# Kernel tuning notes

Hardware: AMD Instinct MI355X
Metric: run time of the kernel (lower is better)

The kernel has to match this reference:

```python
import jax, jax.numpy as jnp
import numpy as np

T = 256          # total_sequence_length
COND = 192       # condition_size
H = 256          # latent_size
B = 4096         # batch
MEAN = 0.0
STD = 1.0


def setup_inputs() -> dict:
    key = jax.random.key(0)
    ks = jax.random.split(key, 8)
    s = 1.0 / np.sqrt(H)  # PyTorch RNN init scale
    return {
        "cd": jax.random.normal(ks[0], (B, COND), dtype=jnp.float32),
        "prediction": jax.random.normal(ks[1], (B, T - COND), dtype=jnp.float32),
        "w_ih": jax.random.uniform(ks[2], (4 * H, 1), jnp.float32, -s, s),
        "w_hh": jax.random.uniform(ks[3], (4 * H, H), jnp.float32, -s, s),
        "b_ih": jax.random.uniform(ks[4], (4 * H,), jnp.float32, -s, s),
        "b_hh": jax.random.uniform(ks[5], (4 * H,), jnp.float32, -s, s),
        "w_out": jax.random.uniform(ks[6], (1, H), jnp.float32, -s, s),
        "b_out": jax.random.uniform(ks[7], (1,), jnp.float32, -s, s),
    }


def reference(cd, prediction, w_ih, w_hh, b_ih, b_hh, w_out, b_out):
    # concat condition + prediction -> [B, T], normalize
    d_input = jnp.concatenate([cd, prediction.reshape(-1, T - COND)], axis=1)
    d_input = (d_input - MEAN) / STD
    # time-major [T, B]; input_size=1 so x-projection is an outer product
    x = d_input.T  # [T, B]
    # precompute input gates for all timesteps: [T, B, 4H]
    x_gates = x[:, :, None] * w_ih[:, 0][None, None, :] + b_ih

    def step(carry, xg):
        h, c = carry
        gates = xg + h @ w_hh.T + b_hh  # [B, 4H]
        i, f, g, o = jnp.split(gates, 4, axis=1)
        i = jax.nn.sigmoid(i)
        f = jax.nn.sigmoid(f)
        g = jnp.tanh(g)
        o = jax.nn.sigmoid(o)
        c = f * c + i * g
        h = o * jnp.tanh(c)
        return (h, c), None

    h0 = jnp.zeros((B, H), dtype=cd.dtype)
    c0 = jnp.zeros((B, H), dtype=cd.dtype)
    (h_last, _), _ = jax.lax.scan(step, (h0, c0), x_gates)
    # trailing linear + sigmoid on last hidden state -> [B, 1]
    return jax.nn.sigmoid(h_last @ w_out.T + b_out)
```

## Files before the change

kernel.cpp:

```cpp
#include <hip/hip_runtime.h>

#define TT 256
#define CONDL 192
#define PREDL 64
#define HH 256
#define BB 4096
#define BT 16
#define NTHR 1024

#define WSC 2032.0f
#define HSC 127.0f
#define SINV (1.0f / (127.0f * 2032.0f))
#define L2E 1.44269504f
#define CSX (-L2E * SINV)
#define CGX (2.0f * L2E * SINV)

typedef int i32x4 __attribute__((ext_vector_type(4)));
typedef signed char i8x16 __attribute__((ext_vector_type(16)));
typedef unsigned short u16x4 __attribute__((ext_vector_type(4)));

__device__ __forceinline__ short f2bf(float f) {
  unsigned u = __builtin_bit_cast(unsigned, f);
  unsigned r = (u + 0x7fffu + ((u >> 16) & 1u)) >> 16;
  return (short)r;
}
__device__ __forceinline__ float bf2f(short s) {
  unsigned u = ((unsigned)(unsigned short)s) << 16;
  return __builtin_bit_cast(float, u);
}
__device__ __forceinline__ float sig_(float x) {
  return __builtin_amdgcn_rcpf(1.0f + __builtin_amdgcn_exp2f(-L2E * x));
}

__global__ void pack_w(const float* __restrict__ w_hh, signed char* __restrict__ wq) {
  int idx = blockIdx.x * 256 + threadIdx.x;
  int lane = idx & 63;
  int kb = (idx >> 6) & 3;
  int jt = idx >> 8;
  int n = jt * 16 + (lane & 15);
  int k0 = kb * 64 + (lane >> 4) * 16;
  i8x16 v;
#pragma unroll
  for (int j = 0; j < 16; ++j)
    v[j] = (signed char)__float2int_rn(w_hh[n * 256 + k0 + j] * WSC);
  *(i8x16*)(wq + (long)idx * 16) = v;
}

__global__ __launch_bounds__(NTHR, 4)
void lstm_main(const float* __restrict__ cd, const float* __restrict__ pred,
               const float* __restrict__ w_ih, const float* __restrict__ b_ih,
               const float* __restrict__ b_hh, const float* __restrict__ w_out,
               const float* __restrict__ b_out, const signed char* __restrict__ wq,
               float* __restrict__ out) {
  __shared__ __align__(16) signed char h_s[2 * 4096];
  __shared__ __align__(16) short x_s[TT * BT];

  const int tid = threadIdx.x;
  const int lane = tid & 63;
  const int wv = tid >> 6;
  const int r0 = blockIdx.x * BT;
  const int lm = lane & 15;
  const int lq = lane >> 4;
  const int m0 = lq * 4;

  for (int i = tid; i < BT * CONDL; i += NTHR) {
    int r = i / CONDL, t = i % CONDL;
    x_s[t * BT + r] = f2bf(cd[(r0 + r) * CONDL + t]);
  }
  for (int i = tid; i < BT * PREDL; i += NTHR) {
    int r = i / PREDL, t = i % PREDL;
    x_s[(CONDL + t) * BT + r] = f2bf(pred[(r0 + r) * PREDL + t]);
  }
  for (int i = tid; i < 1024; i += NTHR) ((int*)h_s)[i] = 0;

  const i32x4* wq4 = (const i32x4*)wq;
  i32x4 wrq[16];
#pragma unroll
  for (int g = 0; g < 4; ++g) {
    int jt = g * 16 + wv;
#pragma unroll
    for (int kb = 0; kb < 4; ++kb)
      wrq[g * 4 + kb] = wq4[(jt * 4 + kb) * 64 + lane];
  }
#pragma unroll
  for (int i = 0; i < 16; ++i) asm volatile("" : "+v"(wrq[i]));

  float wf_[4], bf_[4];
#pragma unroll
  for (int g = 0; g < 4; ++g) {
    int j = g * 256 + wv * 16 + lm;
    float fac = (g == 2) ? (2.0f * L2E) : -L2E;
    wf_[g] = w_ih[j] * fac;
    bf_[g] = (b_ih[j] + b_hh[j]) * fac;
  }

  const int wbb = (wv >> 2) * 1024 + (wv & 3) * 256 + lq * 64 + lm;

  float cst[4];
#pragma unroll
  for (int i = 0; i < 4; ++i) cst[i] = 0.f;

  i32x4 zeroi;
  zeroi[0] = 0; zeroi[1] = 0; zeroi[2] = 0; zeroi[3] = 0;

  __syncthreads();

  for (int t = 0; t < TT; ++t) {
    const signed char* hr = h_s + (t & 1) * 4096;
    signed char* hw = h_s + ((t + 1) & 1) * 4096;

    i32x4 acc[4];

    i32x4 af_c = *(const i32x4*)(hr + lane * 16);
#pragma unroll
    for (int kb = 0; kb < 4; ++kb) {
      i32x4 af = af_c;
      if (kb < 3) af_c = *(const i32x4*)(hr + (kb + 1) * 1024 + lane * 16);
      acc[0] = __builtin_amdgcn_mfma_i32_16x16x64_i8(
          af, wrq[0 * 4 + kb], kb ? acc[0] : zeroi, 0, 0, 0);
      acc[1] = __builtin_amdgcn_mfma_i32_16x16x64_i8(
          af, wrq[1 * 4 + kb], kb ? acc[1] : zeroi, 0, 0, 0);
      acc[2] = __builtin_amdgcn_mfma_i32_16x16x64_i8(
          af, wrq[2 * 4 + kb], kb ? acc[2] : zeroi, 0, 0, 0);
      acc[3] = __builtin_amdgcn_mfma_i32_16x16x64_i8(
          af, wrq[3 * 4 + kb], kb ? acc[3] : zeroi, 0, 0, 0);
    }

    u16x4 xq = *(const u16x4*)(x_s + t * BT + m0);
    float xr[4];
#pragma unroll
    for (int v = 0; v < 4; ++v) xr[v] = bf2f((short)xq[v]);

#pragma unroll
    for (int v = 0; v < 4; ++v) {
      float aI = (float)acc[0][v];
      float aF = (float)acc[1][v];
      float aG = (float)acc[2][v];
      float aO = (float)acc[3][v];
      float xi = xr[v];
      float eI = __builtin_amdgcn_exp2f(fmaf(aI, CSX, fmaf(xi, wf_[0], bf_[0])));
      float eF = __builtin_amdgcn_exp2f(fmaf(aF, CSX, fmaf(xi, wf_[1], bf_[1])));
      float eG = __builtin_amdgcn_exp2f(fmaf(aG, CGX, fmaf(xi, wf_[2], bf_[2])));
      float eO = __builtin_amdgcn_exp2f(fmaf(aO, CSX, fmaf(xi, wf_[3], bf_[3])));
      float A_ = 1.0f + eI, F_ = 1.0f + eF, G_ = 1.0f + eG, O_ = 1.0f + eO;
      float AG = A_ * G_;
      float num = fmaf(G_ - 2.0f, F_, cst[v] * AG);
      float r1 = __builtin_amdgcn_rcpf(F_ * AG);
      float cn = num * r1;
      cst[v] = cn;
      float eC = __builtin_amdgcn_exp2f(fminf(cn * (2.0f * L2E), 126.0f));
      float C2 = 1.0f + eC;
      float r2 = __builtin_amdgcn_rcpf(O_ * C2);
      float h127 = fmaf(HSC, C2, -2.0f * HSC) * r2;
      hw[wbb + v * 16] = (signed char)__float2int_rn(h127);
    }
    __syncthreads();
  }

  const signed char* hf = h_s;
  float bo = b_out[0];
  {
    int row = wv;
    float p = 0.f;
#pragma unroll
    for (int c = 0; c < 4; ++c) {
      int k = lane + c * 64;
      int idx = c * 1024 + ((lane >> 4) & 3) * 256 + row * 16 + (lane & 15);
      p += (float)hf[idx] * w_out[k];
    }
#pragma unroll
    for (int off = 32; off > 0; off >>= 1) p += __shfl_down(p, off);
    if (lane == 0) out[r0 + row] = sig_(p * (1.0f / HSC) + bo);
  }
}

extern "C" void kernel_launch(void* const* d_in, const int* in_sizes, int n_in,
                              void* d_out, int out_size, void* d_ws, size_t ws_size,
                              hipStream_t stream) {
  const float* cd    = (const float*)d_in[0];
  const float* pr    = (const float*)d_in[1];
  const float* w_ih  = (const float*)d_in[2];
  const float* w_hh  = (const float*)d_in[3];
  const float* b_ih  = (const float*)d_in[4];
  const float* b_hh  = (const float*)d_in[5];
  const float* w_out = (const float*)d_in[6];
  const float* b_out = (const float*)d_in[7];
  float* out = (float*)d_out;
  signed char* wp = (signed char*)d_ws;

  pack_w<<<64, 256, 0, stream>>>(w_hh, wp);
  lstm_main<<<256, NTHR, 0, stream>>>(cd, pr, w_ih, b_ih, b_hh, w_out, b_out, wp, out);
}
```

Before: 418.8 us.

## Fold input projection and bias into int8 MFMA as extra K block, overlap exp with MFMA

Adds a fifth K block to the int8 MFMA: the quantized input x (replicated 8 times) and a constant 127 column multiply packed w_ih and bias weights, so the gate pre-activations arrive fully formed from the matrix unit. The per-element input FMAs and bias handling are removed from the recurrent step. The MFMA chain is split into two halves so the sigmoid exponentials for the i and f gates can run while the g and o MFMAs are still executing. This costs 25% more MFMA work and coarse int8 quantization of the input (scale 24, clipped) and of the bias, which can reduce accuracy.

```diff
diff --git a/kernel.cpp b/kernel.cpp
--- a/kernel.cpp
+++ b/kernel.cpp
@@ -14,10 +14,13 @@
 #define L2E 1.44269504f
 #define CSX (-L2E * SINV)
 #define CGX (2.0f * L2E * SINV)
+#define XQS 24.0f
+#define WXS (258064.0f / (XQS * 8.0f))
+#define WBS 1016.0f
+#define HB 5120
 
 typedef int i32x4 __attribute__((ext_vector_type(4)));
 typedef signed char i8x16 __attribute__((ext_vector_type(16)));
-typedef unsigned short u16x4 __attribute__((ext_vector_type(4)));
 
 __device__ __forceinline__ short f2bf(float f) {
   unsigned u = __builtin_bit_cast(unsigned, f);
@@ -32,28 +35,41 @@
   return __builtin_amdgcn_rcpf(1.0f + __builtin_amdgcn_exp2f(-L2E * x));
 }
 
-__global__ void pack_w(const float* __restrict__ w_hh, signed char* __restrict__ wq) {
+__global__ void pack_w(const float* __restrict__ w_hh, const float* __restrict__ w_ih,
+                       const float* __restrict__ b_ih, const float* __restrict__ b_hh,
+                       signed char* __restrict__ wq) {
   int idx = blockIdx.x * 256 + threadIdx.x;
   int lane = idx & 63;
-  int kb = (idx >> 6) & 3;
-  int jt = idx >> 8;
+  int f = idx >> 6;
+  int kb = f % 5;
+  int jt = f / 5;
   int n = jt * 16 + (lane & 15);
-  int k0 = kb * 64 + (lane >> 4) * 16;
+  int lq = lane >> 4;
   i8x16 v;
-#pragma unroll
-  for (int j = 0; j < 16; ++j)
-    v[j] = (signed char)__float2int_rn(w_hh[n * 256 + k0 + j] * WSC);
+  if (kb < 4) {
+    int k0 = kb * 64 + lq * 16;
+#pragma unroll
+    for (int j = 0; j < 16; ++j)
+      v[j] = (signed char)__float2int_rn(w_hh[n * 256 + k0 + j] * WSC);
+  } else {
+    signed char wx = 0, wb = 0;
+    if (lq == 0) {
+      wx = (signed char)__float2int_rn(w_ih[n] * WXS);
+      wb = (signed char)__float2int_rn((b_ih[n] + b_hh[n]) * WBS);
+    }
+#pragma unroll
+    for (int j = 0; j < 16; ++j)
+      v[j] = (j < 8) ? wx : ((j < 10) ? wb : (signed char)0);
+  }
   *(i8x16*)(wq + (long)idx * 16) = v;
 }
 
 __global__ __launch_bounds__(NTHR, 4)
 void lstm_main(const float* __restrict__ cd, const float* __restrict__ pred,
-               const float* __restrict__ w_ih, const float* __restrict__ b_ih,
-               const float* __restrict__ b_hh, const float* __restrict__ w_out,
-               const float* __restrict__ b_out, const signed char* __restrict__ wq,
-               float* __restrict__ out) {
-  __shared__ __align__(16) signed char h_s[2 * 4096];
-  __shared__ __align__(16) short x_s[TT * BT];
+               const float* __restrict__ w_out, const float* __restrict__ b_out,
+               const signed char* __restrict__ wq, float* __restrict__ out) {
+  __shared__ __align__(16) signed char h_s[2 * HB];
+  __shared__ __align__(16) short x_s[(TT + 1) * BT];
 
   const int tid = threadIdx.x;
   const int lane = tid & 63;
@@ -61,7 +77,6 @@
   const int r0 = blockIdx.x * BT;
   const int lm = lane & 15;
   const int lq = lane >> 4;
-  const int m0 = lq * 4;
 
   for (int i = tid; i < BT * CONDL; i += NTHR) {
     int r = i / CONDL, t = i % CONDL;
@@ -71,28 +86,20 @@
     int r = i / PREDL, t = i % PREDL;
     x_s[(CONDL + t) * BT + r] = f2bf(pred[(r0 + r) * PREDL + t]);
   }
-  for (int i = tid; i < 1024; i += NTHR) ((int*)h_s)[i] = 0;
+  for (int i = tid; i < BT; i += NTHR) x_s[TT * BT + i] = 0;
+  for (int i = tid; i < (2 * HB) / 4; i += NTHR) ((int*)h_s)[i] = 0;
 
   const i32x4* wq4 = (const i32x4*)wq;
-  i32x4 wrq[16];
+  i32x4 wrq[20];
 #pragma unroll
   for (int g = 0; g < 4; ++g) {
     int jt = g * 16 + wv;
 #pragma unroll
-    for (int kb = 0; kb < 4; ++kb)
-      wrq[g * 4 + kb] = wq4[(jt * 4 + kb) * 64 + lane];
-  }
-#pragma unroll
-  for (int i = 0; i < 16; ++i) asm volatile("" : "+v"(wrq[i]));
-
-  float wf_[4], bf_[4];
-#pragma unroll
-  for (int g = 0; g < 4; ++g) {
-    int j = g * 256 + wv * 16 + lm;
-    float fac = (g == 2) ? (2.0f * L2E) : -L2E;
-    wf_[g] = w_ih[j] * fac;
-    bf_[g] = (b_ih[j] + b_hh[j]) * fac;
-  }
+    for (int kb = 0; kb < 5; ++kb)
+      wrq[g * 5 + kb] = wq4[(jt * 5 + kb) * 64 + lane];
+  }
+#pragma unroll
+  for (int i = 0; i < 20; ++i) asm volatile("" : "+v"(wrq[i]));
 
   const int wbb = (wv >> 2) * 1024 + (wv & 3) * 256 + lq * 64 + lm;
 
@@ -105,44 +112,82 @@
 
   __syncthreads();
 
+  if (lane == 0) {
+    *(short*)(h_s + 0 * HB + 4096 + wv * 16 + 8) = 0x7F7F;
+    *(short*)(h_s + 1 * HB + 4096 + wv * 16 + 8) = 0x7F7F;
+    float xv = cd[(r0 + wv) * CONDL];
+    float xc = __builtin_amdgcn_fmed3f(xv * XQS, -127.0f, 127.0f);
+    unsigned b = (unsigned)__float2int_rn(xc) & 0xffu;
+    unsigned d = b * 0x01010101u;
+    *(unsigned*)(h_s + 4096 + wv * 16) = d;
+    *(unsigned*)(h_s + 4096 + wv * 16 + 4) = d;
+  }
+  __syncthreads();
+
   for (int t = 0; t < TT; ++t) {
-    const signed char* hr = h_s + (t & 1) * 4096;
-    signed char* hw = h_s + ((t + 1) & 1) * 4096;
-
-    i32x4 acc[4];
-
-    i32x4 af_c = *(const i32x4*)(hr + lane * 16);
-#pragma unroll
-    for (int kb = 0; kb < 4; ++kb) {
-      i32x4 af = af_c;
-      if (kb < 3) af_c = *(const i32x4*)(hr + (kb + 1) * 1024 + lane * 16);
-      acc[0] = __builtin_amdgcn_mfma_i32_16x16x64_i8(
-          af, wrq[0 * 4 + kb], kb ? acc[0] : zeroi, 0, 0, 0);
-      acc[1] = __builtin_amdgcn_mfma_i32_16x16x64_i8(
-          af, wrq[1 * 4 + kb], kb ? acc[1] : zeroi, 0, 0, 0);
-      acc[2] = __builtin_amdgcn_mfma_i32_16x16x64_i8(
-          af, wrq[2 * 4 + kb], kb ? acc[2] : zeroi, 0, 0, 0);
-      acc[3] = __builtin_amdgcn_mfma_i32_16x16x64_i8(
-          af, wrq[3 * 4 + kb], kb ? acc[3] : zeroi, 0, 0, 0);
-    }
-
-    u16x4 xq = *(const u16x4*)(x_s + t * BT + m0);
-    float xr[4];
-#pragma unroll
-    for (int v = 0; v < 4; ++v) xr[v] = bf2f((short)xq[v]);
-
+    const signed char* hr = h_s + (t & 1) * HB;
+    signed char* hw = h_s + ((t + 1) & 1) * HB;
+
+    i32x4 acc0, acc1, acc2, acc3;
+
+    {
+      i32x4 afc = *(const i32x4*)(hr + lane * 16);
+#pragma unroll
+      for (int kb = 0; kb < 5; ++kb) {
+        i32x4 af = afc;
+        if (kb < 4) afc = *(const i32x4*)(hr + (kb + 1) * 1024 + lane * 16);
+        acc0 = __builtin_amdgcn_mfma_i32_16x16x64_i8(
+            af, wrq[0 + kb], kb ? acc0 : zeroi, 0, 0, 0);
+        acc1 = __builtin_amdgcn_mfma_i32_16x16x64_i8(
+            af, wrq[5 + kb], kb ? acc1 : zeroi, 0, 0, 0);
+      }
+    }
+
+    float eI[4], eF[4], eG[4], eO[4];
+
+    {
+      i32x4 afc = *(const i32x4*)(hr + lane * 16);
+#pragma unroll
+      for (int kb = 0; kb < 5; ++kb) {
+        i32x4 af = afc;
+        if (kb < 4) afc = *(const i32x4*)(hr + (kb + 1) * 1024 + lane * 16);
+        acc2 = __builtin_amdgcn_mfma_i32_16x16x64_i8(
+            af, wrq[10 + kb], kb ? acc2 : zeroi, 0, 0, 0);
+        acc3 = __builtin_amdgcn_mfma_i32_16x16x64_i8(
+            af, wrq[15 + kb], kb ? acc3 : zeroi, 0, 0, 0);
+        if (kb == 1) {
+          eI[0] = __builtin_amdgcn_exp2f((float)acc0[0] * CSX);
+          eI[1] = __builtin_amdgcn_exp2f((float)acc0[1] * CSX);
+        } else if (kb == 2) {
+          eI[2] = __builtin_amdgcn_exp2f((float)acc0[2] * CSX);
+          eI[3] = __builtin_amdgcn_exp2f((float)acc0[3] * CSX);
+        } else if (kb == 3) {
+          eF[0] = __builtin_amdgcn_exp2f((float)acc1[0] * CSX);
+          eF[1] = __builtin_amdgcn_exp2f((float)acc1[1] * CSX);
+        } else if (kb == 4) {
+          eF[2] = __builtin_amdgcn_exp2f((float)acc1[2] * CSX);
+          eF[3] = __builtin_amdgcn_exp2f((float)acc1[3] * CSX);
+        }
+      }
+    }
 #pragma unroll
     for (int v = 0; v < 4; ++v) {
-      float aI = (float)acc[0][v];
-      float aF = (float)acc[1][v];
-      float aG = (float)acc[2][v];
-      float aO = (float)acc[3][v];
-      float xi = xr[v];
-      float eI = __builtin_amdgcn_exp2f(fmaf(aI, CSX, fmaf(xi, wf_[0], bf_[0])));
-      float eF = __builtin_amdgcn_exp2f(fmaf(aF, CSX, fmaf(xi, wf_[1], bf_[1])));
-      float eG = __builtin_amdgcn_exp2f(fmaf(aG, CGX, fmaf(xi, wf_[2], bf_[2])));
-      float eO = __builtin_amdgcn_exp2f(fmaf(aO, CSX, fmaf(xi, wf_[3], bf_[3])));
-      float A_ = 1.0f + eI, F_ = 1.0f + eF, G_ = 1.0f + eG, O_ = 1.0f + eO;
+      eG[v] = __builtin_amdgcn_exp2f((float)acc2[v] * CGX);
+      eO[v] = __builtin_amdgcn_exp2f((float)acc3[v] * CSX);
+    }
+
+    if (lane == 0) {
+      float xv = bf2f(x_s[(t + 1) * BT + wv]);
+      float xc = __builtin_amdgcn_fmed3f(xv * XQS, -127.0f, 127.0f);
+      unsigned b = (unsigned)__float2int_rn(xc) & 0xffu;
+      unsigned d = b * 0x01010101u;
+      *(unsigned*)(hw + 4096 + wv * 16) = d;
+      *(unsigned*)(hw + 4096 + wv * 16 + 4) = d;
+    }
+
+#pragma unroll
+    for (int v = 0; v < 4; ++v) {
+      float A_ = 1.0f + eI[v], F_ = 1.0f + eF[v], G_ = 1.0f + eG[v], O_ = 1.0f + eO[v];
       float AG = A_ * G_;
       float num = fmaf(G_ - 2.0f, F_, cst[v] * AG);
       float r1 = __builtin_amdgcn_rcpf(F_ * AG);
@@ -188,6 +233,6 @@
   float* out = (float*)d_out;
   signed char* wp = (signed char*)d_ws;
 
-  pack_w<<<64, 256, 0, stream>>>(w_hh, wp);
-  lstm_main<<<256, NTHR, 0, stream>>>(cd, pr, w_ih, b_ih, b_hh, w_out, b_out, wp, out);
-}
+  pack_w<<<80, 256, 0, stream>>>(w_hh, w_ih, b_ih, b_hh, wp);
+  lstm_main<<<256, NTHR, 0, stream>>>(cd, pr, w_out, b_out, wp, out);
+}
```

After: 451.2 us. 1.08x slower.
